# Kernel optimization log

Measured on AMD Instinct MI355X. Metric: run time of the kernel, lower is better.

## Reference

```python
import jax, jax.numpy as jnp
import numpy as np

RATIOS = (2, 2, 2)
IN_SIZE = 512
DATA_SIZE = 2
NOISE_BANDS = 5
TARGET_SIZE = int(np.prod(RATIOS))  # 8


def conv1d(x, w, b, stride):
    # cc.get_padding(3, stride, mode='centered'): total pad = 3 - stride = 1 -> (left, right) = (0, 1)
    y = jax.lax.conv_general_dilated(
        x, w, window_strides=(stride,), padding=[(0, 1)],
        dimension_numbers=('NCH', 'OIH', 'NCH'))
    return y + b[None, :, None]


def mod_sigmoid(x):
    return 2.0 * jax.nn.sigmoid(x) ** 2.3 + 1e-7


def amp_to_impulse_response(amp, target_size):
    # amp: [..., noise_bands] real, treated as complex spectrum with zero imag
    ir = jnp.fft.irfft(amp)                      # [..., 2*(nb-1)]
    fs = ir.shape[-1]
    ir = jnp.roll(ir, fs // 2, axis=-1)
    n = jnp.arange(fs, dtype=ir.dtype)
    win = 0.5 * (1.0 - jnp.cos(2.0 * jnp.pi * n / fs))  # periodic hann (torch default)
    ir = ir * win
    pad = int(target_size) - fs                   # 0 for our config
    ir = jnp.pad(ir, [(0, 0)] * (ir.ndim - 1) + [(0, pad)])
    return jnp.roll(ir, -(fs // 2), axis=-1)


def fft_convolve(signal, kernel):
    n = signal.shape[-1]
    pad_cfg = [(0, 0)] * (signal.ndim - 1)
    s = jnp.pad(signal, pad_cfg + [(0, n)])
    k = jnp.pad(kernel, pad_cfg + [(n, 0)])
    out = jnp.fft.irfft(jnp.fft.rfft(s) * jnp.fft.rfft(k))
    return out[..., out.shape[-1] // 2:]


def setup_inputs() -> dict:
    key = jax.random.key(0)
    ks = jax.random.split(key, 8)
    B, T = 16, 4096
    c_out = DATA_SIZE * NOISE_BANDS
    x = jax.random.normal(ks[0], (B, IN_SIZE, T), dtype=jnp.float32)
    noise = jax.random.uniform(ks[1], (B, T // TARGET_SIZE, DATA_SIZE, TARGET_SIZE), dtype=jnp.float32)
    w1 = jax.random.normal(ks[2], (IN_SIZE, IN_SIZE, 3), dtype=jnp.float32) * 0.03
    b1 = jnp.zeros((IN_SIZE,), dtype=jnp.float32)
    w2 = jax.random.normal(ks[3], (IN_SIZE, IN_SIZE, 3), dtype=jnp.float32) * 0.03
    b2 = jnp.zeros((IN_SIZE,), dtype=jnp.float32)
    w3 = jax.random.normal(ks[4], (c_out, IN_SIZE, 3), dtype=jnp.float32) * 0.03
    b3 = jnp.zeros((c_out,), dtype=jnp.float32)
    return {"x": x, "noise": noise, "w1": w1, "b1": b1, "w2": w2, "b2": b2, "w3": w3, "b3": b3}


def reference(x, noise, w1, b1, w2, b2, w3, b3):
    h = conv1d(x, w1, b1, RATIOS[0])
    h = jax.nn.leaky_relu(h, 0.2)
    h = conv1d(h, w2, b2, RATIOS[1])
    h = jax.nn.leaky_relu(h, 0.2)
    h = conv1d(h, w3, b3, RATIOS[2])            # [B, data_size*nb, T']
    amp = mod_sigmoid(h - 5.0)
    amp = jnp.transpose(amp, (0, 2, 1))          # [B, T', data_size*nb]
    B, Tp = amp.shape[0], amp.shape[1]
    amp = amp.reshape(B, Tp, DATA_SIZE, -1)      # [B, T', data_size, nb]
    ir = amp_to_impulse_response(amp, TARGET_SIZE)  # [B, T', data_size, target]
    nz = noise * 2.0 - 1.0                        # torch.rand_like(ir)*2-1
    out = fft_convolve(nz, ir)                    # [B, T', data_size, target]
    out = jnp.transpose(out, (0, 2, 1, 3))        # [B, data_size, T', target]
    return out.reshape(B, DATA_SIZE, -1)          # [B, data_size, T'*target]
```

## Files before the change

### kernel.cpp

```cpp
#include <hip/hip_runtime.h>
#include <math.h>


typedef __attribute__((ext_vector_type(8)))  short bf16x8;
typedef __attribute__((ext_vector_type(16))) float f32x16;

__device__ __forceinline__ unsigned short f2bf_rne(float f) {
    unsigned int u = __float_as_uint(f);
    unsigned int r = u + 0x7fff + ((u >> 16) & 1);
    return (unsigned short)(r >> 16);
}
__device__ __forceinline__ float bf2f(unsigned short h) {
    return __uint_as_float(((unsigned int)h) << 16);
}
__device__ __forceinline__ void gload_lds16(const void* g, void* l) {
    __builtin_amdgcn_global_load_lds(
        (const __attribute__((address_space(1))) unsigned int*)g,
        (__attribute__((address_space(3))) unsigned int*)l, 16, 0, 0);
}

__global__ void prep_x_kernel(const float* __restrict__ X, char* __restrict__ Xt)
{
    __shared__ float tile[256][33];
    const int t0  = blockIdx.x * 32;
    const int ch  = blockIdx.y;
    const int b   = blockIdx.z;
    const int tid = threadIdx.x;

    const float* xb = X + ((size_t)b * 512 + (size_t)ch * 256) * 4096;
#pragma unroll
    for (int i = 0; i < 32; ++i) {
        int idx = i * 256 + tid;
        int ci = idx >> 5, tl = idx & 31;
        tile[ci][tl] = xb[(size_t)ci * 4096 + t0 + tl];
    }
    __syncthreads();
    char* ob = Xt + ((size_t)b * 4128 + t0) * 2048 + ch * 512;
#pragma unroll
    for (int i = 0; i < 64; ++i) {
        int idx = i * 256 + tid;
        int hl  = idx >> 13;
        int rem = idx & 8191;
        int tl = rem >> 8, ci = rem & 255;
        float v = tile[ci][tl];
        unsigned short hi = f2bf_rne(v);
        unsigned short val = hl ? f2bf_rne(v - bf2f(hi)) : hi;
        *(unsigned short*)(ob + (size_t)tl * 2048 + hl * 1024 + ci * 2) = val;
    }
}

__global__ void prep_w_kernel(const float* __restrict__ W, short* __restrict__ Wf)
{
    int gid = blockIdx.x * 256 + threadIdx.x;
    int f = gid >> 6, l = gid & 63;
    int ks = f & 1, hl = (f >> 1) & 1;
    int k  = (f >> 2) % 3;
    int rem = (f >> 2) / 3;
    int cob = rem & 15, cb = rem >> 4;
    int co  = cob * 32 + (l & 31);
    int ci0 = cb * 32 + ks * 16 + (l >> 5) * 8;
    bf16x8 o;
#pragma unroll
    for (int j = 0; j < 8; ++j) {
        float v = W[((size_t)co * 512 + ci0 + j) * 3 + k];
        unsigned short hi = f2bf_rne(v);
        o[j] = hl ? (short)f2bf_rne(v - bf2f(hi)) : (short)hi;
    }
    *(bf16x8*)((char*)Wf + (size_t)f * 1024 + l * 16) = o;
}

__global__ void zero_pads1(char* __restrict__ xt, char* __restrict__ h1p) {
    int id = blockIdx.x * 256 + threadIdx.x;
    if (id < 16384) {
        int b = id >> 10, w = id & 1023;
        *(float*)(xt + ((size_t)b * 4128 + 4096) * 2048 + (size_t)w * 4) = 0.f;
    } else {
        int id2 = id - 16384;
        int b = id2 >> 10, w = id2 & 1023;
        *(float*)(h1p + ((size_t)b * 2080 + 2048) * 2048 + (size_t)w * 4) = 0.f;
    }
}
__global__ void zero_pads2(char* __restrict__ h2t) {
    int id = blockIdx.x * 256 + threadIdx.x;
    int b = id >> 10, w = id & 1023;
    *(float*)(h2t + ((size_t)b * 1026 + 1024) * 2048 + (size_t)w * 4) = 0.f;
}

#define CONV_UNITS 1032

__global__ __launch_bounds__(256, 2) void conv_mfma(
    const char* __restrict__ Xp, const short* __restrict__ Wf,
    const float* __restrict__ Bias, char* __restrict__ Out,
    int rowsX, int rowsO, int Yt, int mode)
{
    __shared__ char AB[2][16512];

    const int tid = threadIdx.x;
    const int l   = tid & 63;
    const int wid = tid >> 6;
    const int tl0 = l & 31;
    const int lh  = l >> 5;

    int p = blockIdx.x;
    int chunk = p >> 5, slot = p & 31;
    int gl = slot & 15, c = slot >> 4;
    int g = chunk * 16 + gl;
    int zb = g / Yt, y = g - zb * Yt;

    const int bt0 = y * 64;
    const int r0  = 2 * bt0;
    const char* Xb = Xp + (size_t)zb * (size_t)rowsX * 2048;

    f32x16 acc[2][2];
#pragma unroll
    for (int tp = 0; tp < 2; ++tp)
#pragma unroll
        for (int cp = 0; cp < 2; ++cp) acc[tp][cp] = (f32x16)(0.0f);

    const int cbase = c * 8 + wid * 2;

    auto stage = [&](char* buf, int cb) {
#pragma unroll
        for (int i = 0; i < 5; ++i) {
            int u = i * 256 + tid;
            if (u < CONV_UNITS) {
                int r = u >> 3, ul = u & 7;
                int us = ul ^ ((r >> 1) & 7);
                const char* gp = Xb + (size_t)(r0 + r) * 2048
                               + (us >> 2) * 1024 + cb * 64 + (us & 3) * 16;
                gload_lds16(gp, buf + ((size_t)(i * 256 + wid * 64)) * 16);
            }
        }
    };

    stage(AB[0], 0);
    __syncthreads();

    for (int cb = 0; cb < 16; ++cb) {
        if (cb < 15) stage(AB[(cb + 1) & 1], cb + 1);
        const char* Ab = AB[cb & 1];
#pragma unroll
        for (int ph = 0; ph < 6; ++ph) {
            const int tap = ph >> 1, ks = ph & 1;
            bf16x8 a[2][2], bb[2][2];
#pragma unroll
            for (int tp = 0; tp < 2; ++tp) {
                int rl = 2 * (tp * 32 + tl0) + tap;
                int sw = (rl >> 1) & 7;
                int qb = ks * 2 + lh;
                a[0][tp] = *(const bf16x8*)(Ab + rl * 128 + ((qb ^ sw) << 4));
                a[1][tp] = *(const bf16x8*)(Ab + rl * 128 + (((qb + 4) ^ sw) << 4));
            }
#pragma unroll
            for (int cp = 0; cp < 2; ++cp) {
                size_t f0 = ((((size_t)(cb * 16 + cbase + cp) * 3 + tap) * 2 + 0) * 2 + ks);
                const char* wp = (const char*)Wf + f0 * 1024 + l * 16;
                bb[0][cp] = *(const bf16x8*)(wp);
                bb[1][cp] = *(const bf16x8*)(wp + 2048);
            }
#pragma unroll
            for (int tp = 0; tp < 2; ++tp)
#pragma unroll
                for (int cp = 0; cp < 2; ++cp) {
                    acc[tp][cp] = __builtin_amdgcn_mfma_f32_32x32x16_bf16(
                        a[0][tp], bb[0][cp], acc[tp][cp], 0, 0, 0);
                    acc[tp][cp] = __builtin_amdgcn_mfma_f32_32x32x16_bf16(
                        a[0][tp], bb[1][cp], acc[tp][cp], 0, 0, 0);
                    acc[tp][cp] = __builtin_amdgcn_mfma_f32_32x32x16_bf16(
                        a[1][tp], bb[0][cp], acc[tp][cp], 0, 0, 0);
                }
        }
        __syncthreads();
    }

    const size_t outB = (size_t)zb * (size_t)rowsO * 2048;
    const int colb = c * 256 + wid * 64 + tl0;
#pragma unroll
    for (int cp = 0; cp < 2; ++cp) {
        int co = colb + cp * 32;
        float bv = Bias[co];
#pragma unroll
        for (int tp = 0; tp < 2; ++tp) {
            int trow = bt0 + tp * 32 + 4 * lh;
#pragma unroll
            for (int r = 0; r < 16; ++r) {
                int row = trow + (r & 3) + 8 * (r >> 2);
                float v = acc[tp][cp][r] + bv;
                v = v < 0.f ? 0.2f * v : v;
                char* po = Out + outB + (size_t)row * 2048;
                if (mode == 0) {
                    unsigned short hi = f2bf_rne(v);
                    unsigned short lo = f2bf_rne(v - bf2f(hi));
                    *(unsigned short*)(po + co * 2) = hi;
                    *(unsigned short*)(po + 1024 + co * 2) = lo;
                } else {
                    *(float*)(po + (size_t)co * 4) = v;
                }
            }
        }
    }
}

__global__ __launch_bounds__(256) void conv3_tmaj(
    const float* __restrict__ H2, const float* __restrict__ W3,
    const float* __restrict__ B3, const float* __restrict__ Noise,
    float* __restrict__ Out)
{
    __shared__ float W3s[1536][10];
    __shared__ float Xe[32][40];
    __shared__ float Xo[32][40];
    __shared__ float hs[32][12];

    const int b   = blockIdx.y;
    const int t0  = blockIdx.x * 32;
    const int tid = threadIdx.x;
    const int t   = tid & 31;
    const int gch = tid >> 5;

    for (int idx = tid; idx < 15360; idx += 256) {
        int co = idx / 1536;
        int r  = idx - co * 1536;
        W3s[r][co] = W3[idx];
    }

    float acc3[2] = {0.f, 0.f};
    const float* Hb = H2 + (size_t)b * 1026 * 512;

    for (int c0 = 0; c0 < 512; c0 += 32) {
        __syncthreads();
        for (int idx = tid; idx < 33 * 32; idx += 256) {
            int pp = idx >> 5, ci = idx & 31;
            Xe[ci][pp] = Hb[(size_t)(2 * t0 + 2 * pp) * 512 + c0 + ci];
            Xo[ci][pp] = Hb[(size_t)(2 * t0 + 2 * pp + 1) * 512 + c0 + ci];
        }
        __syncthreads();

        for (int ci = 0; ci < 32; ++ci) {
            float xe0 = Xe[ci][t];
            float xo0 = Xo[ci][t];
            float xe1 = Xe[ci][t + 1];
            int r = (c0 + ci) * 3;
#pragma unroll
            for (int m = 0; m < 2; ++m) {
                int cc = gch + m * 8;
                if (cc < 10) {
                    acc3[m] = fmaf(W3s[r][cc], xe0,
                              fmaf(W3s[r + 1][cc], xo0,
                              fmaf(W3s[r + 2][cc], xe1, acc3[m])));
                }
            }
        }
    }

#pragma unroll
    for (int m = 0; m < 2; ++m) {
        int cc = gch + m * 8;
        if (cc < 10) hs[t][cc] = acc3[m] + B3[cc];
    }
    __syncthreads();

    if (tid < 64) {
        const int tt = tid & 31;
        const int d  = tid >> 5;

        float A[5];
#pragma unroll
        for (int j = 0; j < 5; ++j) {
            float h = hs[tt][d * 5 + j] - 5.f;
            float s = 1.f / (1.f + expf(-h));
            A[j] = 2.f * powf(s, 2.3f) + 1e-7f;
        }

        const float SQ = 0.70710678118654752f;
        const float c1[8] = {1.f, SQ, 0.f, -SQ, -1.f, -SQ, 0.f, SQ};
        const float c2[8] = {1.f, 0.f, -1.f, 0.f, 1.f, 0.f, -1.f, 0.f};
        const float c3[8] = {1.f, -SQ, 0.f, SQ, -1.f, SQ, 0.f, -SQ};
        const float c4[8] = {1.f, -1.f, 1.f, -1.f, 1.f, -1.f, 1.f, -1.f};
        const float wsh[8] = {1.f, 0.85355339059327376f, 0.5f, 0.14644660940672624f,
                              0.f, 0.14644660940672624f, 0.5f, 0.85355339059327376f};

        float ir[8];
#pragma unroll
        for (int n = 0; n < 8; ++n) {
            float v = A[0] + 2.f * (A[1] * c1[n] + A[2] * c2[n] + A[3] * c3[n])
                    + A[4] * c4[n];
            ir[n] = 0.125f * v * wsh[n];
        }

        const float* npi = Noise + (size_t)b * 8192 + (size_t)(t0 + tt) * 16 + d * 8;
        float nz[8];
#pragma unroll
        for (int j = 0; j < 8; ++j) nz[j] = 2.f * npi[j] - 1.f;

        float* op = Out + (size_t)b * 8192 + (size_t)d * 4096 + (size_t)(t0 + tt) * 8;
#pragma unroll
        for (int o = 0; o < 8; ++o) {
            float s = 0.f;
#pragma unroll
            for (int j = 0; j <= o; ++j) s += nz[j] * ir[o - j];
            op[o] = s;
        }
    }
}

#define BCO 64
#define BT  128
#define KC  16

__global__ __launch_bounds__(256, 2) void conv_s2_kernel(
    const float* __restrict__ X, const float* __restrict__ W,
    const float* __restrict__ Bias, float* __restrict__ Y,
    int Cin, int Tin, int Cout, int Tout, int leaky)
{
    __shared__ float Xe[KC][132];
    __shared__ float Xo[KC][132];
    __shared__ float Wk[KC * 3][68];

    const int b   = blockIdx.z;
    const int co0 = blockIdx.y * BCO;
    const int t0  = blockIdx.x * BT;
    const int tid = threadIdx.x;
    const int ty  = tid & 15;
    const int tx  = tid >> 4;

    const float* Xb = X + (size_t)b * Cin * Tin;

    float acc[4][8];
#pragma unroll
    for (int i = 0; i < 4; ++i)
#pragma unroll
        for (int j = 0; j < 8; ++j) acc[i][j] = 0.f;

    for (int c0 = 0; c0 < Cin; c0 += KC) {
        __syncthreads();
        for (int idx = tid; idx < KC * 130; idx += 256) {
            int ci = idx / 130;
            int pp = idx - ci * 130;
            int gt = 2 * t0 + 2 * pp;
            const float* src = Xb + (size_t)(c0 + ci) * Tin;
            float e, o;
            if (gt + 1 < Tin) {
                float2 v = *(const float2*)(src + gt);
                e = v.x; o = v.y;
            } else {
                e = (gt < Tin) ? src[gt] : 0.f;
                o = 0.f;
            }
            Xe[ci][pp] = e;
            Xo[ci][pp] = o;
        }
        {
            const float* Wc = W + (size_t)co0 * Cin * 3 + (size_t)c0 * 3;
            for (int idx = tid; idx < BCO * (KC * 3); idx += 256) {
                int co = idx / 48;
                int r  = idx - co * 48;
                Wk[r][co] = Wc[(size_t)co * Cin * 3 + r];
            }
        }
        __syncthreads();

#pragma unroll
        for (int ci = 0; ci < KC; ++ci) {
            float4 xe0 = *(const float4*)&Xe[ci][tx * 8];
            float4 xe1 = *(const float4*)&Xe[ci][tx * 8 + 4];
            float  xe8 = Xe[ci][tx * 8 + 8];
            float4 xo0 = *(const float4*)&Xo[ci][tx * 8];
            float4 xo1 = *(const float4*)&Xo[ci][tx * 8 + 4];
            float4 w0  = *(const float4*)&Wk[ci * 3 + 0][ty * 4];
            float4 w1  = *(const float4*)&Wk[ci * 3 + 1][ty * 4];
            float4 w2  = *(const float4*)&Wk[ci * 3 + 2][ty * 4];
            float xe[9] = {xe0.x, xe0.y, xe0.z, xe0.w, xe1.x, xe1.y, xe1.z, xe1.w, xe8};
            float xo[8] = {xo0.x, xo0.y, xo0.z, xo0.w, xo1.x, xo1.y, xo1.z, xo1.w};
            float wa[3][4] = {{w0.x, w0.y, w0.z, w0.w},
                              {w1.x, w1.y, w1.z, w1.w},
                              {w2.x, w2.y, w2.z, w2.w}};
#pragma unroll
            for (int i = 0; i < 4; ++i)
#pragma unroll
                for (int j = 0; j < 8; ++j)
                    acc[i][j] = fmaf(wa[0][i], xe[j],
                                fmaf(wa[1][i], xo[j],
                                fmaf(wa[2][i], xe[j + 1], acc[i][j])));
        }
    }

    float* Yb = Y + (size_t)b * Cout * Tout;
#pragma unroll
    for (int i = 0; i < 4; ++i) {
        int   co = co0 + ty * 4 + i;
        float bv = Bias[co];
        float ov[8];
#pragma unroll
        for (int j = 0; j < 8; ++j) {
            float v = acc[i][j] + bv;
            ov[j] = (leaky && v < 0.f) ? 0.2f * v : v;
        }
        float* dst = Yb + (size_t)co * Tout + t0 + tx * 8;
        *(float4*)dst       = make_float4(ov[0], ov[1], ov[2], ov[3]);
        *(float4*)(dst + 4) = make_float4(ov[4], ov[5], ov[6], ov[7]);
    }
}

__global__ __launch_bounds__(256) void conv3_cmaj(
    const float* __restrict__ H2, const float* __restrict__ W3,
    const float* __restrict__ B3, const float* __restrict__ Noise,
    float* __restrict__ Out)
{
    __shared__ float W3s[1536][10];
    __shared__ float Xe[32][40];
    __shared__ float Xo[32][40];
    __shared__ float hs[32][12];

    const int b   = blockIdx.y;
    const int t0  = blockIdx.x * 32;
    const int tid = threadIdx.x;
    const int t   = tid & 31;
    const int gch = tid >> 5;

    for (int idx = tid; idx < 15360; idx += 256) {
        int co = idx / 1536;
        int r  = idx - co * 1536;
        W3s[r][co] = W3[idx];
    }

    float acc3[2] = {0.f, 0.f};
    const float* Hb = H2 + (size_t)b * 512 * 1024;

    for (int c0 = 0; c0 < 512; c0 += 32) {
        __syncthreads();
        for (int idx = tid; idx < 32 * 33; idx += 256) {
            int ci = idx / 33;
            int pp = idx - ci * 33;
            int gt = 2 * t0 + 2 * pp;
            const float* src = Hb + (size_t)(c0 + ci) * 1024;
            float e, o;
            if (gt + 1 < 1024) {
                float2 v = *(const float2*)(src + gt);
                e = v.x; o = v.y;
            } else {
                e = (gt < 1024) ? src[gt] : 0.f;
                o = 0.f;
            }
            Xe[ci][pp] = e;
            Xo[ci][pp] = o;
        }
        __syncthreads();

        for (int ci = 0; ci < 32; ++ci) {
            float xe0 = Xe[ci][t];
            float xo0 = Xo[ci][t];
            float xe1 = Xe[ci][t + 1];
            int r = (c0 + ci) * 3;
#pragma unroll
            for (int m = 0; m < 2; ++m) {
                int cc = gch + m * 8;
                if (cc < 10)
                    acc3[m] = fmaf(W3s[r][cc], xe0,
                              fmaf(W3s[r + 1][cc], xo0,
                              fmaf(W3s[r + 2][cc], xe1, acc3[m])));
            }
        }
    }

#pragma unroll
    for (int m = 0; m < 2; ++m) {
        int cc = gch + m * 8;
        if (cc < 10) hs[t][cc] = acc3[m] + B3[cc];
    }
    __syncthreads();

    if (tid < 64) {
        const int tt = tid & 31;
        const int d  = tid >> 5;
        float A[5];
#pragma unroll
        for (int j = 0; j < 5; ++j) {
            float h = hs[tt][d * 5 + j] - 5.f;
            float s = 1.f / (1.f + expf(-h));
            A[j] = 2.f * powf(s, 2.3f) + 1e-7f;
        }
        const float SQ = 0.70710678118654752f;
        const float c1[8] = {1.f, SQ, 0.f, -SQ, -1.f, -SQ, 0.f, SQ};
        const float c2[8] = {1.f, 0.f, -1.f, 0.f, 1.f, 0.f, -1.f, 0.f};
        const float c3[8] = {1.f, -SQ, 0.f, SQ, -1.f, SQ, 0.f, -SQ};
        const float c4[8] = {1.f, -1.f, 1.f, -1.f, 1.f, -1.f, 1.f, -1.f};
        const float wsh[8] = {1.f, 0.85355339059327376f, 0.5f, 0.14644660940672624f,
                              0.f, 0.14644660940672624f, 0.5f, 0.85355339059327376f};
        float ir[8];
#pragma unroll
        for (int n = 0; n < 8; ++n) {
            float v = A[0] + 2.f * (A[1] * c1[n] + A[2] * c2[n] + A[3] * c3[n])
                    + A[4] * c4[n];
            ir[n] = 0.125f * v * wsh[n];
        }
        const float* npi = Noise + (size_t)b * 8192 + (size_t)(t0 + tt) * 16 + d * 8;
        float nz[8];
#pragma unroll
        for (int j = 0; j < 8; ++j) nz[j] = 2.f * npi[j] - 1.f;
        float* op = Out + (size_t)b * 8192 + (size_t)d * 4096 + (size_t)(t0 + tt) * 8;
#pragma unroll
        for (int o = 0; o < 8; ++o) {
            float s = 0.f;
#pragma unroll
            for (int j = 0; j <= o; ++j) s += nz[j] * ir[o - j];
            op[o] = s;
        }
    }
}

extern "C" void kernel_launch(void* const* d_in, const int* in_sizes, int n_in,
                              void* d_out, int out_size, void* d_ws, size_t ws_size,
                              hipStream_t stream) {
    const float* x     = (const float*)d_in[0];
    const float* noise = (const float*)d_in[1];
    const float* w1    = (const float*)d_in[2];
    const float* b1    = (const float*)d_in[3];
    const float* w2    = (const float*)d_in[4];
    const float* b2    = (const float*)d_in[5];
    const float* w3    = (const float*)d_in[6];
    const float* b3    = (const float*)d_in[7];
    float* out = (float*)d_out;

    const size_t XT_BYTES  = (size_t)16 * 4128 * 2048;
    const size_t H1P_BYTES = (size_t)16 * 2080 * 2048;
    const size_t WF_BYTES  = (size_t)512 * 512 * 3 * 2 * 2;
    const size_t NEED = XT_BYTES + H1P_BYTES + 2 * WF_BYTES;

    if (ws_size >= NEED) {
        char*  xt  = (char*)d_ws;
        char*  h1p = xt + XT_BYTES;
        short* Wf1 = (short*)(h1p + H1P_BYTES);
        short* Wf2 = (short*)((char*)Wf1 + WF_BYTES);
        char*  h2t = xt;

        prep_x_kernel<<<dim3(128, 2, 16), 256, 0, stream>>>(x, xt);
        prep_w_kernel<<<768, 256, 0, stream>>>(w1, Wf1);
        prep_w_kernel<<<768, 256, 0, stream>>>(w2, Wf2);
        zero_pads1<<<128, 256, 0, stream>>>(xt, h1p);
        conv_mfma<<<1024, 256, 0, stream>>>(xt, Wf1, b1, h1p, 4128, 2080, 32, 0);
        zero_pads2<<<64, 256, 0, stream>>>(h2t);
        conv_mfma<<<512, 256, 0, stream>>>(h1p, Wf2, b2, h2t, 2080, 1026, 16, 1);
        conv3_tmaj<<<dim3(16, 16), 256, 0, stream>>>((const float*)h2t, w3, b3, noise, out);
    } else {
        float* h1 = (float*)d_ws;
        float* h2 = h1 + (size_t)16 * 512 * 2048;
        dim3 blk(256);
        conv_s2_kernel<<<dim3(2048 / BT, 512 / BCO, 16), blk, 0, stream>>>(
            x, w1, b1, h1, 512, 4096, 512, 2048, 1);
        conv_s2_kernel<<<dim3(1024 / BT, 512 / BCO, 16), blk, 0, stream>>>(
            h1, w2, b2, h2, 512, 2048, 512, 1024, 1);
        conv3_cmaj<<<dim3(16, 16), blk, 0, stream>>>(h2, w3, b3, noise, out);
    }
}
```

Before: 368.6 us.

## Fuse input transpose and bf16 split into first conv kernel

Removes the separate prep_x kernel that transposed x into time-major hi/lo bf16 layout. The first conv now loads fp32 x directly from global memory, splits each value into hi and lo bf16 halves in registers, and writes them into a swizzled LDS tile, double-buffered across channel blocks. This drops a full write and re-read of a ~270MB intermediate and one launch. In exchange the conv does strided loads and conversion arithmetic inside its main loop, and the two pad-zeroing kernels are merged into one.

```diff
diff --git a/kernel.cpp b/kernel.cpp
--- a/kernel.cpp
+++ b/kernel.cpp
@@ -18,35 +18,8 @@
         (const __attribute__((address_space(1))) unsigned int*)g,
         (__attribute__((address_space(3))) unsigned int*)l, 16, 0, 0);
 }
-
-__global__ void prep_x_kernel(const float* __restrict__ X, char* __restrict__ Xt)
-{
-    __shared__ float tile[256][33];
-    const int t0  = blockIdx.x * 32;
-    const int ch  = blockIdx.y;
-    const int b   = blockIdx.z;
-    const int tid = threadIdx.x;
-
-    const float* xb = X + ((size_t)b * 512 + (size_t)ch * 256) * 4096;
-#pragma unroll
-    for (int i = 0; i < 32; ++i) {
-        int idx = i * 256 + tid;
-        int ci = idx >> 5, tl = idx & 31;
-        tile[ci][tl] = xb[(size_t)ci * 4096 + t0 + tl];
-    }
-    __syncthreads();
-    char* ob = Xt + ((size_t)b * 4128 + t0) * 2048 + ch * 512;
-#pragma unroll
-    for (int i = 0; i < 64; ++i) {
-        int idx = i * 256 + tid;
-        int hl  = idx >> 13;
-        int rem = idx & 8191;
-        int tl = rem >> 8, ci = rem & 255;
-        float v = tile[ci][tl];
-        unsigned short hi = f2bf_rne(v);
-        unsigned short val = hl ? f2bf_rne(v - bf2f(hi)) : hi;
-        *(unsigned short*)(ob + (size_t)tl * 2048 + hl * 1024 + ci * 2) = val;
-    }
+__device__ __forceinline__ int swz1(int r) {
+    return ((r >> 1) ^ (r >> 4)) & 7;
 }
 
 __global__ void prep_w_kernel(const float* __restrict__ W, short* __restrict__ Wf)
@@ -69,21 +42,161 @@
     *(bf16x8*)((char*)Wf + (size_t)f * 1024 + l * 16) = o;
 }
 
-__global__ void zero_pads1(char* __restrict__ xt, char* __restrict__ h1p) {
+__global__ void zero_pads(char* __restrict__ h1p, char* __restrict__ h2t) {
     int id = blockIdx.x * 256 + threadIdx.x;
     if (id < 16384) {
         int b = id >> 10, w = id & 1023;
-        *(float*)(xt + ((size_t)b * 4128 + 4096) * 2048 + (size_t)w * 4) = 0.f;
+        *(float*)(h1p + ((size_t)b * 2080 + 2048) * 2048 + (size_t)w * 4) = 0.f;
     } else {
         int id2 = id - 16384;
         int b = id2 >> 10, w = id2 & 1023;
-        *(float*)(h1p + ((size_t)b * 2080 + 2048) * 2048 + (size_t)w * 4) = 0.f;
-    }
-}
-__global__ void zero_pads2(char* __restrict__ h2t) {
-    int id = blockIdx.x * 256 + threadIdx.x;
-    int b = id >> 10, w = id & 1023;
-    *(float*)(h2t + ((size_t)b * 1026 + 1024) * 2048 + (size_t)w * 4) = 0.f;
+        *(float*)(h2t + ((size_t)b * 1026 + 1024) * 2048 + (size_t)w * 4) = 0.f;
+    }
+}
+
+__global__ __launch_bounds__(256, 2) void conv1_fused(
+    const float* __restrict__ X, const short* __restrict__ Wf,
+    const float* __restrict__ Bias, char* __restrict__ Out)
+{
+    __shared__ char AB[2][16512];
+
+    const int tid = threadIdx.x;
+    const int l   = tid & 63;
+    const int wid = tid >> 6;
+    const int tl0 = l & 31;
+    const int lh  = l >> 5;
+
+    int p = blockIdx.x;
+    int chunk = p >> 5, slot = p & 31;
+    int gl = slot & 15, c = slot >> 4;
+    int g = chunk * 16 + gl;
+    int zb = g >> 5, y = g & 31;
+
+    const int bt0 = y * 64;
+    const int r0  = 2 * bt0;
+    const float* Xb = X + (size_t)zb * 512 * 4096;
+
+    const int rg  = tid & 15;
+    const int cip = tid >> 4;
+
+    f32x16 acc[2][2];
+#pragma unroll
+    for (int tp = 0; tp < 2; ++tp)
+#pragma unroll
+        for (int cp = 0; cp < 2; ++cp) acc[tp][cp] = (f32x16)(0.0f);
+
+    const int cbase = c * 8 + wid * 2;
+
+    float4 fx0, fx1, fx2, fx3;
+    float  fextra = 0.f;
+
+    auto issue_loads = [&](int cb) {
+        const float* s0 = Xb + (size_t)(cb * 32 + 2 * cip) * 4096 + r0 + rg * 8;
+        fx0 = *(const float4*)(s0);
+        fx1 = *(const float4*)(s0 + 4);
+        fx2 = *(const float4*)(s0 + 4096);
+        fx3 = *(const float4*)(s0 + 4100);
+        if (tid < 32) {
+            int rr = r0 + 128;
+            fextra = (rr < 4096) ? Xb[(size_t)(cb * 32 + tid) * 4096 + rr] : 0.f;
+        }
+    };
+
+    auto write_tile = [&](char* buf) {
+        float va[8] = {fx0.x, fx0.y, fx0.z, fx0.w, fx1.x, fx1.y, fx1.z, fx1.w};
+        float vb[8] = {fx2.x, fx2.y, fx2.z, fx2.w, fx3.x, fx3.y, fx3.z, fx3.w};
+        const int ci   = 2 * cip;
+        const int u_hi = ci >> 3;
+        const int u_lo = 4 + u_hi;
+        const int coff = (ci & 7) * 2;
+#pragma unroll
+        for (int k = 0; k < 8; ++k) {
+            int r  = rg * 8 + k;
+            int sw = swz1(r);
+            unsigned short h0 = f2bf_rne(va[k]);
+            unsigned short l0 = f2bf_rne(va[k] - bf2f(h0));
+            unsigned short h1 = f2bf_rne(vb[k]);
+            unsigned short l1 = f2bf_rne(vb[k] - bf2f(h1));
+            *(unsigned int*)(buf + r * 128 + (((u_hi ^ sw)) << 4) + coff) =
+                (unsigned int)h0 | ((unsigned int)h1 << 16);
+            *(unsigned int*)(buf + r * 128 + (((u_lo ^ sw)) << 4) + coff) =
+                (unsigned int)l0 | ((unsigned int)l1 << 16);
+        }
+        if (tid < 32) {
+            int sw = swz1(128);
+            unsigned short h = f2bf_rne(fextra);
+            unsigned short lo = f2bf_rne(fextra - bf2f(h));
+            int uh = (tid >> 3) ^ sw;
+            int ul = (4 + (tid >> 3)) ^ sw;
+            *(unsigned short*)(buf + 128 * 128 + (uh << 4) + (tid & 7) * 2) = h;
+            *(unsigned short*)(buf + 128 * 128 + (ul << 4) + (tid & 7) * 2) = lo;
+        }
+    };
+
+    issue_loads(0);
+    write_tile(AB[0]);
+    __syncthreads();
+
+    for (int cb = 0; cb < 16; ++cb) {
+        if (cb < 15) issue_loads(cb + 1);
+        const char* Ab = AB[cb & 1];
+#pragma unroll
+        for (int ph = 0; ph < 6; ++ph) {
+            const int tap = ph >> 1, ks = ph & 1;
+            bf16x8 a[2][2], bb[2][2];
+#pragma unroll
+            for (int tp = 0; tp < 2; ++tp) {
+                int rl = 2 * (tp * 32 + tl0) + tap;
+                int sw = swz1(rl);
+                int qb = ks * 2 + lh;
+                a[0][tp] = *(const bf16x8*)(Ab + rl * 128 + ((qb ^ sw) << 4));
+                a[1][tp] = *(const bf16x8*)(Ab + rl * 128 + (((qb + 4) ^ sw) << 4));
+            }
+#pragma unroll
+            for (int cp = 0; cp < 2; ++cp) {
+                size_t f0 = ((((size_t)(cb * 16 + cbase + cp) * 3 + tap) * 2 + 0) * 2 + ks);
+                const char* wp = (const char*)Wf + f0 * 1024 + l * 16;
+                bb[0][cp] = *(const bf16x8*)(wp);
+                bb[1][cp] = *(const bf16x8*)(wp + 2048);
+            }
+#pragma unroll
+            for (int tp = 0; tp < 2; ++tp)
+#pragma unroll
+                for (int cp = 0; cp < 2; ++cp) {
+                    acc[tp][cp] = __builtin_amdgcn_mfma_f32_32x32x16_bf16(
+                        a[0][tp], bb[0][cp], acc[tp][cp], 0, 0, 0);
+                    acc[tp][cp] = __builtin_amdgcn_mfma_f32_32x32x16_bf16(
+                        a[0][tp], bb[1][cp], acc[tp][cp], 0, 0, 0);
+                    acc[tp][cp] = __builtin_amdgcn_mfma_f32_32x32x16_bf16(
+                        a[1][tp], bb[0][cp], acc[tp][cp], 0, 0, 0);
+                }
+        }
+        if (cb < 15) write_tile(AB[(cb + 1) & 1]);
+        __syncthreads();
+    }
+
+    const size_t outB = (size_t)zb * 2080 * 2048;
+    const int colb = c * 256 + wid * 64 + tl0;
+#pragma unroll
+    for (int cp = 0; cp < 2; ++cp) {
+        int co = colb + cp * 32;
+        float bv = Bias[co];
+#pragma unroll
+        for (int tp = 0; tp < 2; ++tp) {
+            int trow = bt0 + tp * 32 + 4 * lh;
+#pragma unroll
+            for (int r = 0; r < 16; ++r) {
+                int row = trow + (r & 3) + 8 * (r >> 2);
+                float v = acc[tp][cp][r] + bv;
+                v = v < 0.f ? 0.2f * v : v;
+                char* po = Out + outB + (size_t)row * 2048;
+                unsigned short hi = f2bf_rne(v);
+                unsigned short lo = f2bf_rne(v - bf2f(hi));
+                *(unsigned short*)(po + co * 2) = hi;
+                *(unsigned short*)(po + 1024 + co * 2) = lo;
+            }
+        }
+    }
 }
 
 #define CONV_UNITS 1032
@@ -521,24 +634,21 @@
     const float* b3    = (const float*)d_in[7];
     float* out = (float*)d_out;
 
-    const size_t XT_BYTES  = (size_t)16 * 4128 * 2048;
     const size_t H1P_BYTES = (size_t)16 * 2080 * 2048;
+    const size_t H2T_BYTES = (size_t)16 * 1026 * 512 * 4;
     const size_t WF_BYTES  = (size_t)512 * 512 * 3 * 2 * 2;
-    const size_t NEED = XT_BYTES + H1P_BYTES + 2 * WF_BYTES;
+    const size_t NEED = H1P_BYTES + H2T_BYTES + 2 * WF_BYTES;
 
     if (ws_size >= NEED) {
-        char*  xt  = (char*)d_ws;
-        char*  h1p = xt + XT_BYTES;
-        short* Wf1 = (short*)(h1p + H1P_BYTES);
+        char*  h1p = (char*)d_ws;
+        char*  h2t = h1p + H1P_BYTES;
+        short* Wf1 = (short*)(h2t + H2T_BYTES);
         short* Wf2 = (short*)((char*)Wf1 + WF_BYTES);
-        char*  h2t = xt;
-
-        prep_x_kernel<<<dim3(128, 2, 16), 256, 0, stream>>>(x, xt);
+
         prep_w_kernel<<<768, 256, 0, stream>>>(w1, Wf1);
         prep_w_kernel<<<768, 256, 0, stream>>>(w2, Wf2);
-        zero_pads1<<<128, 256, 0, stream>>>(xt, h1p);
-        conv_mfma<<<1024, 256, 0, stream>>>(xt, Wf1, b1, h1p, 4128, 2080, 32, 0);
-        zero_pads2<<<64, 256, 0, stream>>>(h2t);
+        zero_pads<<<128, 256, 0, stream>>>(h1p, h2t);
+        conv1_fused<<<1024, 256, 0, stream>>>(x, Wf1, b1, h1p);
         conv_mfma<<<512, 256, 0, stream>>>(h1p, Wf2, b2, h2t, 2080, 1026, 16, 1);
         conv3_tmaj<<<dim3(16, 16), 256, 0, stream>>>((const float*)h2t, w3, b3, noise, out);
     } else {
```

Result: faster. 317.5 us (-13.9%).
